# Performance work log

Measured on AMD Instinct MI355X. Metric: run time of the kernel, lower is better.

The kernel has to match this reference:

```python
import jax, jax.numpy as jnp
import numpy as np

N = 50000
E = 600000
D_IN = 128
D_OUT = 128


def setup_inputs() -> dict:
    key = jax.random.key(0)
    k1, k2, k3 = jax.random.split(key, 3)
    x = jax.random.normal(k1, (N, D_IN), dtype=jnp.float32)
    edge_index = jax.random.randint(k2, (2, E), 0, N, dtype=jnp.int64)
    W = jax.random.normal(k3, (D_IN, D_OUT), dtype=jnp.float32) / np.sqrt(D_IN)
    b = jnp.zeros((D_OUT,), dtype=jnp.float32)
    return {"x": x, "edge_index": edge_index, "W": W, "b": b}


def reference(x, edge_index, W, b):
    n = x.shape[0]
    # add self-loops (PyG GCNConv default add_self_loops=True)
    loop = jnp.arange(n, dtype=edge_index.dtype)
    src = jnp.concatenate([edge_index[0], loop])  # message sources
    dst = jnp.concatenate([edge_index[1], loop])  # aggregation targets

    # linear transform first (small GEMM), then normalized aggregation
    h = x @ W  # [N, D_OUT]

    ones = jnp.ones(src.shape[0], dtype=x.dtype)
    deg = jax.ops.segment_sum(ones, dst, num_segments=n)  # in-degree incl. self-loop
    dis = jnp.where(deg > 0, jax.lax.rsqrt(jnp.maximum(deg, 1.0)), 0.0)
    norm = dis[src] * dis[dst]  # [E+N]

    msg = h[src] * norm[:, None]  # gather + scale, memory-bound
    out = jax.ops.segment_sum(msg, dst, num_segments=n)  # scatter-add
    return out + b
```

## Files before the change

### kernel.cpp

```cpp
#include <hip/hip_runtime.h>

#define D 128
#define CAP 1024
#define NBMAX 1024
#define EPB 1024

typedef short bf16x8 __attribute__((ext_vector_type(8)));
typedef float f32x4 __attribute__((ext_vector_type(4)));

__device__ __forceinline__ unsigned bf16_rne(float f) {
    unsigned u = __float_as_uint(f);
    unsigned r = u + 0x7FFFu + ((u >> 16) & 1u);
    return r >> 16;
}

__device__ __forceinline__ void bf16_split(float f, short& hi, short& lo) {
    unsigned h = bf16_rne(f);
    float hf = __uint_as_float(h << 16);
    hi = (short)h;
    lo = (short)bf16_rne(f - hf);
}

__device__ __forceinline__ unsigned pk2(float lo, float hi) {
    return bf16_rne(lo) | (bf16_rne(hi) << 16);
}

__device__ __forceinline__ float lo16(unsigned u) { return __uint_as_float(u << 16); }
__device__ __forceinline__ float hi16(unsigned u) { return __uint_as_float(u & 0xFFFF0000u); }

__global__ __launch_bounds__(256) void bin_kernel(const int* __restrict__ ei,
                                                  unsigned* __restrict__ bins,
                                                  int* __restrict__ bcnt, int E, int NB) {
    __shared__ unsigned staged[EPB];
    __shared__ unsigned short bmap[EPB];
    __shared__ int loff[NBMAX + 1];
    __shared__ int lpos[NBMAX];
    __shared__ int lbase[NBMAX];
    __shared__ int wsum[4];
    const int tid = threadIdx.x;
    const int lane = tid & 63, wid = tid >> 6;
    const int base = blockIdx.x * EPB;

    for (int i = tid; i < NBMAX; i += 256) lpos[i] = 0;
    __syncthreads();

    int eb[EPB / 256]; unsigned ev[EPB / 256];
#pragma unroll
    for (int r = 0; r < EPB / 256; ++r) {
        const int idx = base + r * 256 + tid;
        int bkt = -1; unsigned ent = 0;
        if (idx < E) {
            const int s = ei[idx];
            const int d = ei[E + idx];
            bkt = d >> 6;
            ent = (unsigned)s | ((unsigned)(d & 63) << 26);
            atomicAdd(&lpos[bkt], 1);
        }
        eb[r] = bkt; ev[r] = ent;
    }
    __syncthreads();

    {
        const int i0 = tid * 4;
        const int c0 = lpos[i0], c1 = lpos[i0 + 1], c2 = lpos[i0 + 2], c3 = lpos[i0 + 3];
        const int s = c0 + c1 + c2 + c3;
        int sc = s;
#pragma unroll
        for (int o = 1; o < 64; o <<= 1) {
            int t = __shfl_up(sc, o, 64);
            if (lane >= o) sc += t;
        }
        if (lane == 63) wsum[wid] = sc;
        __syncthreads();
        int woff = 0;
#pragma unroll
        for (int w = 0; w < 4; ++w) if (w < wid) woff += wsum[w];
        const int excl = woff + sc - s;
        loff[i0] = excl;
        loff[i0 + 1] = excl + c0;
        loff[i0 + 2] = excl + c0 + c1;
        loff[i0 + 3] = excl + c0 + c1 + c2;
        if (tid == 255) loff[NBMAX] = excl + s;
    }
    __syncthreads();

    for (int i = tid; i < NBMAX; i += 256) {
        const int cnt = loff[i + 1] - loff[i];
        lpos[i] = loff[i];
        lbase[i] = (cnt > 0 && i < NB) ? atomicAdd(&bcnt[i], cnt) : 0;
    }
    __syncthreads();

#pragma unroll
    for (int r = 0; r < EPB / 256; ++r) {
        if (eb[r] >= 0) {
            const int p = atomicAdd(&lpos[eb[r]], 1);
            staged[p] = ev[r];
            bmap[p] = (unsigned short)eb[r];
        }
    }
    __syncthreads();

    const int total = loff[NBMAX];
    for (int slot = tid; slot < total; slot += 256) {
        const int b = bmap[slot];
        const int rel = lbase[b] + (slot - loff[b]);
        if (rel < CAP) bins[(size_t)b * CAP + rel] = staged[slot];
    }
}

__global__ __launch_bounds__(256) void sortdis_kernel(unsigned* __restrict__ bins,
                                                      const int* __restrict__ bcnt,
                                                      int* __restrict__ node_off,
                                                      float* __restrict__ dis, int n) {
    __shared__ unsigned stage[CAP];
    __shared__ unsigned sorted[CAP];
    __shared__ int hist[64], off[65], pos[64];
    const int b = blockIdx.x;
    const int tid = threadIdx.x;
    const int cnt = min(bcnt[b], CAP);
    if (tid < 64) hist[tid] = 0;
    __syncthreads();
    for (int i = tid; i < cnt; i += 256) {
        const unsigned e = bins[(size_t)b * CAP + i];
        stage[i] = e;
        atomicAdd(&hist[e >> 26], 1);
    }
    __syncthreads();
    if (tid < 64) {
        const int v = hist[tid];
        int sc = v;
#pragma unroll
        for (int o = 1; o < 64; o <<= 1) {
            int t = __shfl_up(sc, o, 64);
            if (tid >= o) sc += t;
        }
        off[tid] = sc - v;
        pos[tid] = sc - v;
        if (tid == 63) off[64] = sc;
    }
    __syncthreads();
    for (int i = tid; i < cnt; i += 256) {
        const unsigned e = stage[i];
        const int p = atomicAdd(&pos[e >> 26], 1);
        sorted[p] = e;
    }
    __syncthreads();
    for (int i = tid; i < cnt; i += 256) bins[(size_t)b * CAP + i] = sorted[i];
    if (tid < 65) node_off[b * 65 + tid] = off[tid];
    if (tid < 64) {
        const int node = b * 64 + tid;
        if (node < n) dis[node] = rsqrtf((float)(hist[tid] + 1));
    }
}

__global__ void wprep_kernel(const float* __restrict__ W, short* __restrict__ wh,
                             short* __restrict__ wl) {
    const int t = blockIdx.x * 256 + threadIdx.x;
    if (t >= 8 * 4 * 64) return;
    const int lane = t & 63;
    const int ks = (t >> 6) & 3;
    const int nt = t >> 8;
    const int nn = nt * 16 + (lane & 15);
    const int kbase = ks * 32 + (lane >> 4) * 8;
#pragma unroll
    for (int j = 0; j < 8; ++j) {
        short hi, lo;
        bf16_split(W[(size_t)(kbase + j) * D + nn], hi, lo);
        wh[(size_t)t * 8 + j] = hi;
        wl[(size_t)t * 8 + j] = lo;
    }
}

__global__ __launch_bounds__(256) void gemm_mfma(const float* __restrict__ x,
                                                 const short* __restrict__ wh,
                                                 const short* __restrict__ wl,
                                                 const float* __restrict__ dis,
                                                 unsigned* __restrict__ g, int n) {
    const int wave = threadIdx.x >> 6;
    const int lane = threadIdx.x & 63;
    const int m = lane & 15;
    const int quad = lane >> 4;
    const int row0 = blockIdx.x * 64 + wave * 16;
    const float* xr = x + (size_t)min(row0 + m, n - 1) * D;

    f32x4 acc[8];
#pragma unroll
    for (int nt = 0; nt < 8; ++nt) acc[nt] = (f32x4){0.f, 0.f, 0.f, 0.f};

#pragma unroll
    for (int ks = 0; ks < 4; ++ks) {
        const float4 xa = *(const float4*)&xr[ks * 32 + quad * 8];
        const float4 xb = *(const float4*)&xr[ks * 32 + quad * 8 + 4];
        bf16x8 ah;
        ah[0] = (short)bf16_rne(xa.x);
        ah[1] = (short)bf16_rne(xa.y);
        ah[2] = (short)bf16_rne(xa.z);
        ah[3] = (short)bf16_rne(xa.w);
        ah[4] = (short)bf16_rne(xb.x);
        ah[5] = (short)bf16_rne(xb.y);
        ah[6] = (short)bf16_rne(xb.z);
        ah[7] = (short)bf16_rne(xb.w);
#pragma unroll
        for (int nt = 0; nt < 8; ++nt) {
            const size_t fo = ((size_t)(nt * 4 + ks) * 64 + lane) * 8;
            const bf16x8 bh = *(const bf16x8*)&wh[fo];
            const bf16x8 bl = *(const bf16x8*)&wl[fo];
            acc[nt] = __builtin_amdgcn_mfma_f32_16x16x32_bf16(ah, bh, acc[nt], 0, 0, 0);
            acc[nt] = __builtin_amdgcn_mfma_f32_16x16x32_bf16(ah, bl, acc[nt], 0, 0, 0);
        }
    }

#pragma unroll
    for (int reg = 0; reg < 4; ++reg) {
        const int rr = row0 + quad * 4 + reg;
        if (rr < n) {
            const float dv = dis[rr];
            unsigned* gr = &g[(size_t)rr * 64 + m];
#pragma unroll
            for (int t = 0; t < 4; ++t)
                gr[16 * t] = pk2(acc[t][reg] * dv, acc[t + 4][reg] * dv);
        }
    }
}

__global__ __launch_bounds__(256) void ngather_kernel(const unsigned* __restrict__ bins,
                                                      const int* __restrict__ node_off,
                                                      const float* __restrict__ dis,
                                                      const unsigned* __restrict__ g,
                                                      const float* __restrict__ bvec,
                                                      float* __restrict__ out, int n) {
    const int node = (blockIdx.x * 256 + threadIdx.x) >> 6;
    const int lane = threadIdx.x & 63;
    if (node >= n) return;
    const int b = node >> 6, j = node & 63;
    const int e0 = node_off[b * 65 + j];
    const int e1 = node_off[b * 65 + j + 1];
    const unsigned* bb = bins + (size_t)b * CAP;

    float a0 = 0.f, a1 = 0.f;
    float p0 = 0.f, p1 = 0.f;
    float q0 = 0.f, q1 = 0.f;
    float r0 = 0.f, r1 = 0.f;

    for (int pos = e0; pos < e1; pos += 64) {
        const int mm = min(64, e1 - pos);
        int ent = 0;
        if (lane < mm) ent = (int)bb[pos + lane];
        for (int t = 0; t < mm; t += 16) {
            const int k = mm - t;
            int ss[16];
#pragma unroll
            for (int i = 0; i < 16; ++i)
                ss[i] = __shfl(ent, min(t + i, mm - 1), 64) & 0x03FFFFFF;
            unsigned uu[16];
#pragma unroll
            for (int i = 0; i < 16; ++i)
                uu[i] = g[(size_t)ss[i] * 64 + lane];
#pragma unroll
            for (int i = 0; i < 16; ++i)
                if (i >= k) uu[i] = 0u;
#pragma unroll
            for (int i = 0; i < 16; i += 4) {
                a0 += lo16(uu[i]);     a1 += hi16(uu[i]);
                p0 += lo16(uu[i + 1]); p1 += hi16(uu[i + 1]);
                q0 += lo16(uu[i + 2]); q1 += hi16(uu[i + 2]);
                r0 += lo16(uu[i + 3]); r1 += hi16(uu[i + 3]);
            }
        }
    }
    const unsigned us = g[(size_t)node * 64 + lane];
    a0 += lo16(us) + p0 + q0 + r0;
    a1 += hi16(us) + p1 + q1 + r1;
    const float dv = dis[node];
    out[(size_t)node * D + lane]      = fmaf(dv, a0, bvec[lane]);
    out[(size_t)node * D + lane + 64] = fmaf(dv, a1, bvec[lane + 64]);
}

extern "C" void kernel_launch(void* const* d_in, const int* in_sizes, int n_in,
                              void* d_out, int out_size, void* d_ws, size_t ws_size,
                              hipStream_t stream) {
    const float* x  = (const float*)d_in[0];
    const int*   ei = (const int*)d_in[1];
    const float* W  = (const float*)d_in[2];
    const float* b  = (const float*)d_in[3];
    float* out = (float*)d_out;

    const int n = in_sizes[0] / D;
    const int E = in_sizes[1] / 2;
    const int NB = (n + 63) >> 6;

    char* ws = (char*)d_ws;
    size_t off = 0;
    unsigned* g    = (unsigned*)(ws + off); off += (size_t)n * 64 * sizeof(unsigned);
    float*    dis  = (float*)(ws + off);    off += (size_t)n * sizeof(float);
    unsigned* bins = (unsigned*)(ws + off); off += (size_t)NB * CAP * sizeof(unsigned);
    int*      bcnt = (int*)(ws + off);      off += (size_t)NB * sizeof(int);
    int*  node_off = (int*)(ws + off);      off += (size_t)NB * 65 * sizeof(int);
    short*    wh   = (short*)(ws + off);    off += 8 * 4 * 64 * 8 * sizeof(short);
    short*    wl   = (short*)(ws + off);    off += 8 * 4 * 64 * 8 * sizeof(short);

    hipMemsetAsync(bcnt, 0, (size_t)NB * sizeof(int), stream);

    bin_kernel<<<(E + EPB - 1) / EPB, 256, 0, stream>>>(ei, bins, bcnt, E, NB);
    sortdis_kernel<<<NB, 256, 0, stream>>>(bins, bcnt, node_off, dis, n);
    wprep_kernel<<<8, 256, 0, stream>>>(W, wh, wl);
    gemm_mfma<<<(n + 63) / 64, 256, 0, stream>>>(x, wh, wl, dis, g, n);
    ngather_kernel<<<(n + 3) / 4, 256, 0, stream>>>(bins, node_off, dis, g, b, out, n);
}
```

Measured before the change: 151.9 us.

## Fuse edge binning with GEMM in one launch using separate degree pass

Degrees and dis are now computed by a separate atomic degree kernel, so the GEMM no longer has to wait for the sort kernel. Binning blocks and GEMM blocks are merged into one heterogeneous launch so the two independent stages can run concurrently on the GPU. Edges per bin block grow from 1024 to 4096, which cuts the number of binning blocks and global bcnt atomics. In exchange it adds two small kernels with global atomics on the degree array, and the larger per-block register arrays and shared memory may lower occupancy for the fused kernel.

Result: slower. 161.2 us (+6.2%).

```diff
diff --git a/kernel.cpp b/kernel.cpp
--- a/kernel.cpp
+++ b/kernel.cpp
@@ -3,7 +3,7 @@
 #define D 128
 #define CAP 1024
 #define NBMAX 1024
-#define EPB 1024
+#define EPB 4096
 
 typedef short bf16x8 __attribute__((ext_vector_type(8)));
 typedef float f32x4 __attribute__((ext_vector_type(4)));
@@ -28,9 +28,40 @@
 __device__ __forceinline__ float lo16(unsigned u) { return __uint_as_float(u << 16); }
 __device__ __forceinline__ float hi16(unsigned u) { return __uint_as_float(u & 0xFFFF0000u); }
 
-__global__ __launch_bounds__(256) void bin_kernel(const int* __restrict__ ei,
-                                                  unsigned* __restrict__ bins,
-                                                  int* __restrict__ bcnt, int E, int NB) {
+__global__ void deg_kernel(const int* __restrict__ ei, int* __restrict__ deg, int E) {
+    int e = blockIdx.x * blockDim.x + threadIdx.x;
+    if (e < E) atomicAdd(&deg[ei[E + e]], 1);
+}
+
+__global__ void dis_kernel(const int* __restrict__ deg, float* __restrict__ dis, int n) {
+    int i = blockIdx.x * blockDim.x + threadIdx.x;
+    if (i < n) dis[i] = rsqrtf((float)(deg[i] + 1));
+}
+
+__global__ void wprep_kernel(const float* __restrict__ W, short* __restrict__ wh,
+                             short* __restrict__ wl) {
+    const int t = blockIdx.x * 256 + threadIdx.x;
+    if (t >= 8 * 4 * 64) return;
+    const int lane = t & 63;
+    const int ks = (t >> 6) & 3;
+    const int nt = t >> 8;
+    const int nn = nt * 16 + (lane & 15);
+    const int kbase = ks * 32 + (lane >> 4) * 8;
+#pragma unroll
+    for (int j = 0; j < 8; ++j) {
+        short hi, lo;
+        bf16_split(W[(size_t)(kbase + j) * D + nn], hi, lo);
+        wh[(size_t)t * 8 + j] = hi;
+        wl[(size_t)t * 8 + j] = lo;
+    }
+}
+
+__global__ __launch_bounds__(256) void fused_bin_gemm(
+        const int* __restrict__ ei, unsigned* __restrict__ bins, int* __restrict__ bcnt,
+        int E, int NB, int nbin,
+        const float* __restrict__ x, const short* __restrict__ wh,
+        const short* __restrict__ wl, const float* __restrict__ dis,
+        unsigned* __restrict__ g, int n) {
     __shared__ unsigned staged[EPB];
     __shared__ unsigned short bmap[EPB];
     __shared__ int loff[NBMAX + 1];
@@ -39,80 +70,127 @@
     __shared__ int wsum[4];
     const int tid = threadIdx.x;
     const int lane = tid & 63, wid = tid >> 6;
-    const int base = blockIdx.x * EPB;
-
-    for (int i = tid; i < NBMAX; i += 256) lpos[i] = 0;
-    __syncthreads();
-
-    int eb[EPB / 256]; unsigned ev[EPB / 256];
-#pragma unroll
-    for (int r = 0; r < EPB / 256; ++r) {
-        const int idx = base + r * 256 + tid;
-        int bkt = -1; unsigned ent = 0;
-        if (idx < E) {
-            const int s = ei[idx];
-            const int d = ei[E + idx];
-            bkt = d >> 6;
-            ent = (unsigned)s | ((unsigned)(d & 63) << 26);
-            atomicAdd(&lpos[bkt], 1);
-        }
-        eb[r] = bkt; ev[r] = ent;
-    }
-    __syncthreads();
-
-    {
-        const int i0 = tid * 4;
-        const int c0 = lpos[i0], c1 = lpos[i0 + 1], c2 = lpos[i0 + 2], c3 = lpos[i0 + 3];
-        const int s = c0 + c1 + c2 + c3;
-        int sc = s;
-#pragma unroll
-        for (int o = 1; o < 64; o <<= 1) {
-            int t = __shfl_up(sc, o, 64);
-            if (lane >= o) sc += t;
-        }
-        if (lane == 63) wsum[wid] = sc;
-        __syncthreads();
-        int woff = 0;
-#pragma unroll
-        for (int w = 0; w < 4; ++w) if (w < wid) woff += wsum[w];
-        const int excl = woff + sc - s;
-        loff[i0] = excl;
-        loff[i0 + 1] = excl + c0;
-        loff[i0 + 2] = excl + c0 + c1;
-        loff[i0 + 3] = excl + c0 + c1 + c2;
-        if (tid == 255) loff[NBMAX] = excl + s;
-    }
-    __syncthreads();
-
-    for (int i = tid; i < NBMAX; i += 256) {
-        const int cnt = loff[i + 1] - loff[i];
-        lpos[i] = loff[i];
-        lbase[i] = (cnt > 0 && i < NB) ? atomicAdd(&bcnt[i], cnt) : 0;
-    }
-    __syncthreads();
-
-#pragma unroll
-    for (int r = 0; r < EPB / 256; ++r) {
-        if (eb[r] >= 0) {
-            const int p = atomicAdd(&lpos[eb[r]], 1);
-            staged[p] = ev[r];
-            bmap[p] = (unsigned short)eb[r];
-        }
-    }
-    __syncthreads();
-
-    const int total = loff[NBMAX];
-    for (int slot = tid; slot < total; slot += 256) {
-        const int b = bmap[slot];
-        const int rel = lbase[b] + (slot - loff[b]);
-        if (rel < CAP) bins[(size_t)b * CAP + rel] = staged[slot];
+
+    if ((int)blockIdx.x < nbin) {
+        const int base = blockIdx.x * EPB;
+
+        for (int i = tid; i < NBMAX; i += 256) lpos[i] = 0;
+        __syncthreads();
+
+        int eb[EPB / 256]; unsigned ev[EPB / 256];
+#pragma unroll
+        for (int r = 0; r < EPB / 256; ++r) {
+            const int idx = base + r * 256 + tid;
+            int bkt = -1; unsigned ent = 0;
+            if (idx < E) {
+                const int s = ei[idx];
+                const int d = ei[E + idx];
+                bkt = d >> 6;
+                ent = (unsigned)s | ((unsigned)(d & 63) << 26);
+                atomicAdd(&lpos[bkt], 1);
+            }
+            eb[r] = bkt; ev[r] = ent;
+        }
+        __syncthreads();
+
+        {
+            const int i0 = tid * 4;
+            const int c0 = lpos[i0], c1 = lpos[i0 + 1], c2 = lpos[i0 + 2], c3 = lpos[i0 + 3];
+            const int s = c0 + c1 + c2 + c3;
+            int sc = s;
+#pragma unroll
+            for (int o = 1; o < 64; o <<= 1) {
+                int t = __shfl_up(sc, o, 64);
+                if (lane >= o) sc += t;
+            }
+            if (lane == 63) wsum[wid] = sc;
+            __syncthreads();
+            int woff = 0;
+#pragma unroll
+            for (int w = 0; w < 4; ++w) if (w < wid) woff += wsum[w];
+            const int excl = woff + sc - s;
+            loff[i0] = excl;
+            loff[i0 + 1] = excl + c0;
+            loff[i0 + 2] = excl + c0 + c1;
+            loff[i0 + 3] = excl + c0 + c1 + c2;
+            if (tid == 255) loff[NBMAX] = excl + s;
+        }
+        __syncthreads();
+
+        for (int i = tid; i < NBMAX; i += 256) {
+            const int cnt = loff[i + 1] - loff[i];
+            lpos[i] = loff[i];
+            lbase[i] = (cnt > 0 && i < NB) ? atomicAdd(&bcnt[i], cnt) : 0;
+        }
+        __syncthreads();
+
+#pragma unroll
+        for (int r = 0; r < EPB / 256; ++r) {
+            if (eb[r] >= 0) {
+                const int p = atomicAdd(&lpos[eb[r]], 1);
+                staged[p] = ev[r];
+                bmap[p] = (unsigned short)eb[r];
+            }
+        }
+        __syncthreads();
+
+        const int total = loff[NBMAX];
+        for (int slot = tid; slot < total; slot += 256) {
+            const int b = bmap[slot];
+            const int rel = lbase[b] + (slot - loff[b]);
+            if (rel < CAP) bins[(size_t)b * CAP + rel] = staged[slot];
+        }
+    } else {
+        const int bid = (int)blockIdx.x - nbin;
+        const int m = lane & 15;
+        const int quad = lane >> 4;
+        const int row0 = bid * 64 + wid * 16;
+        const float* xr = x + (size_t)min(row0 + m, n - 1) * D;
+
+        f32x4 acc[8];
+#pragma unroll
+        for (int nt = 0; nt < 8; ++nt) acc[nt] = (f32x4){0.f, 0.f, 0.f, 0.f};
+
+#pragma unroll
+        for (int ks = 0; ks < 4; ++ks) {
+            const float4 xa = *(const float4*)&xr[ks * 32 + quad * 8];
+            const float4 xb = *(const float4*)&xr[ks * 32 + quad * 8 + 4];
+            bf16x8 ah;
+            ah[0] = (short)bf16_rne(xa.x);
+            ah[1] = (short)bf16_rne(xa.y);
+            ah[2] = (short)bf16_rne(xa.z);
+            ah[3] = (short)bf16_rne(xa.w);
+            ah[4] = (short)bf16_rne(xb.x);
+            ah[5] = (short)bf16_rne(xb.y);
+            ah[6] = (short)bf16_rne(xb.z);
+            ah[7] = (short)bf16_rne(xb.w);
+#pragma unroll
+            for (int nt = 0; nt < 8; ++nt) {
+                const size_t fo = ((size_t)(nt * 4 + ks) * 64 + lane) * 8;
+                const bf16x8 bh = *(const bf16x8*)&wh[fo];
+                const bf16x8 bl = *(const bf16x8*)&wl[fo];
+                acc[nt] = __builtin_amdgcn_mfma_f32_16x16x32_bf16(ah, bh, acc[nt], 0, 0, 0);
+                acc[nt] = __builtin_amdgcn_mfma_f32_16x16x32_bf16(ah, bl, acc[nt], 0, 0, 0);
+            }
+        }
+
+#pragma unroll
+        for (int reg = 0; reg < 4; ++reg) {
+            const int rr = row0 + quad * 4 + reg;
+            if (rr < n) {
+                const float dv = dis[rr];
+                unsigned* gr = &g[(size_t)rr * 64 + m];
+#pragma unroll
+                for (int t = 0; t < 4; ++t)
+                    gr[16 * t] = pk2(acc[t][reg] * dv, acc[t + 4][reg] * dv);
+            }
+        }
     }
 }
 
 __global__ __launch_bounds__(256) void sortdis_kernel(unsigned* __restrict__ bins,
                                                       const int* __restrict__ bcnt,
-                                                      int* __restrict__ node_off,
-                                                      float* __restrict__ dis, int n) {
+                                                      int* __restrict__ node_off, int n) {
     __shared__ unsigned stage[CAP];
     __shared__ unsigned sorted[CAP];
     __shared__ int hist[64], off[65], pos[64];
@@ -148,80 +226,6 @@
     __syncthreads();
     for (int i = tid; i < cnt; i += 256) bins[(size_t)b * CAP + i] = sorted[i];
     if (tid < 65) node_off[b * 65 + tid] = off[tid];
-    if (tid < 64) {
-        const int node = b * 64 + tid;
-        if (node < n) dis[node] = rsqrtf((float)(hist[tid] + 1));
-    }
-}
-
-__global__ void wprep_kernel(const float* __restrict__ W, short* __restrict__ wh,
-                             short* __restrict__ wl) {
-    const int t = blockIdx.x * 256 + threadIdx.x;
-    if (t >= 8 * 4 * 64) return;
-    const int lane = t & 63;
-    const int ks = (t >> 6) & 3;
-    const int nt = t >> 8;
-    const int nn = nt * 16 + (lane & 15);
-    const int kbase = ks * 32 + (lane >> 4) * 8;
-#pragma unroll
-    for (int j = 0; j < 8; ++j) {
-        short hi, lo;
-        bf16_split(W[(size_t)(kbase + j) * D + nn], hi, lo);
-        wh[(size_t)t * 8 + j] = hi;
-        wl[(size_t)t * 8 + j] = lo;
-    }
-}
-
-__global__ __launch_bounds__(256) void gemm_mfma(const float* __restrict__ x,
-                                                 const short* __restrict__ wh,
-                                                 const short* __restrict__ wl,
-                                                 const float* __restrict__ dis,
-                                                 unsigned* __restrict__ g, int n) {
-    const int wave = threadIdx.x >> 6;
-    const int lane = threadIdx.x & 63;
-    const int m = lane & 15;
-    const int quad = lane >> 4;
-    const int row0 = blockIdx.x * 64 + wave * 16;
-    const float* xr = x + (size_t)min(row0 + m, n - 1) * D;
-
-    f32x4 acc[8];
-#pragma unroll
-    for (int nt = 0; nt < 8; ++nt) acc[nt] = (f32x4){0.f, 0.f, 0.f, 0.f};
-
-#pragma unroll
-    for (int ks = 0; ks < 4; ++ks) {
-        const float4 xa = *(const float4*)&xr[ks * 32 + quad * 8];
-        const float4 xb = *(const float4*)&xr[ks * 32 + quad * 8 + 4];
-        bf16x8 ah;
-        ah[0] = (short)bf16_rne(xa.x);
-        ah[1] = (short)bf16_rne(xa.y);
-        ah[2] = (short)bf16_rne(xa.z);
-        ah[3] = (short)bf16_rne(xa.w);
-        ah[4] = (short)bf16_rne(xb.x);
-        ah[5] = (short)bf16_rne(xb.y);
-        ah[6] = (short)bf16_rne(xb.z);
-        ah[7] = (short)bf16_rne(xb.w);
-#pragma unroll
-        for (int nt = 0; nt < 8; ++nt) {
-            const size_t fo = ((size_t)(nt * 4 + ks) * 64 + lane) * 8;
-            const bf16x8 bh = *(const bf16x8*)&wh[fo];
-            const bf16x8 bl = *(const bf16x8*)&wl[fo];
-            acc[nt] = __builtin_amdgcn_mfma_f32_16x16x32_bf16(ah, bh, acc[nt], 0, 0, 0);
-            acc[nt] = __builtin_amdgcn_mfma_f32_16x16x32_bf16(ah, bl, acc[nt], 0, 0, 0);
-        }
-    }
-
-#pragma unroll
-    for (int reg = 0; reg < 4; ++reg) {
-        const int rr = row0 + quad * 4 + reg;
-        if (rr < n) {
-            const float dv = dis[rr];
-            unsigned* gr = &g[(size_t)rr * 64 + m];
-#pragma unroll
-            for (int t = 0; t < 4; ++t)
-                gr[16 * t] = pk2(acc[t][reg] * dv, acc[t + 4][reg] * dv);
-        }
-    }
 }
 
 __global__ __launch_bounds__(256) void ngather_kernel(const unsigned* __restrict__ bins,
@@ -289,22 +293,26 @@
     const int n = in_sizes[0] / D;
     const int E = in_sizes[1] / 2;
     const int NB = (n + 63) >> 6;
+    const int nbin = (E + EPB - 1) / EPB;
 
     char* ws = (char*)d_ws;
     size_t off = 0;
     unsigned* g    = (unsigned*)(ws + off); off += (size_t)n * 64 * sizeof(unsigned);
     float*    dis  = (float*)(ws + off);    off += (size_t)n * sizeof(float);
     unsigned* bins = (unsigned*)(ws + off); off += (size_t)NB * CAP * sizeof(unsigned);
+    int*      deg  = (int*)(ws + off);      off += (size_t)n * sizeof(int);
     int*      bcnt = (int*)(ws + off);      off += (size_t)NB * sizeof(int);
     int*  node_off = (int*)(ws + off);      off += (size_t)NB * 65 * sizeof(int);
     short*    wh   = (short*)(ws + off);    off += 8 * 4 * 64 * 8 * sizeof(short);
     short*    wl   = (short*)(ws + off);    off += 8 * 4 * 64 * 8 * sizeof(short);
 
-    hipMemsetAsync(bcnt, 0, (size_t)NB * sizeof(int), stream);
-
-    bin_kernel<<<(E + EPB - 1) / EPB, 256, 0, stream>>>(ei, bins, bcnt, E, NB);
-    sortdis_kernel<<<NB, 256, 0, stream>>>(bins, bcnt, node_off, dis, n);
+    hipMemsetAsync(deg, 0, ((size_t)n + NB) * sizeof(int), stream);
+
+    deg_kernel<<<(E + 255) / 256, 256, 0, stream>>>(ei, deg, E);
+    dis_kernel<<<(n + 255) / 256, 256, 0, stream>>>(deg, dis, n);
     wprep_kernel<<<8, 256, 0, stream>>>(W, wh, wl);
-    gemm_mfma<<<(n + 63) / 64, 256, 0, stream>>>(x, wh, wl, dis, g, n);
+    fused_bin_gemm<<<nbin + (n + 63) / 64, 256, 0, stream>>>(
+        ei, bins, bcnt, E, NB, nbin, x, wh, wl, dis, g, n);
+    sortdis_kernel<<<NB, 256, 0, stream>>>(bins, bcnt, node_off, n);
     ngather_kernel<<<(n + 3) / 4, 256, 0, stream>>>(bins, node_off, dis, g, b, out, n);
 }
```
